# Optimization experiments

Hardware: AMD Instinct MI355X
Metric: run time of the kernel (lower is better)

The kernel has to match this reference:

```python
import jax, jax.numpy as jnp
import numpy as np

BATCH = 2097152
N_BITS = 16

# Differentiable soft gates (exact boolean logic on {0,1} inputs)
def _xor(a, b):
    return a + b - 2.0 * a * b

def _and(a, b):
    return a * b

def _or(a, b):
    return a + b - a * b


def setup_inputs() -> dict:
    key = jax.random.key(0)
    k1, k2 = jax.random.split(key)
    x = jax.random.randint(k1, (BATCH, N_BITS), 0, 2).astype(jnp.float32)
    y = jax.random.randint(k2, (BATCH, N_BITS), 0, 2).astype(jnp.float32)
    return {"x": x, "y": y}


def reference(x, y):
    # Ripple-carry adder: sequential scan over bit positions (LSB first).
    # Full adder with c_in=0 reduces exactly to the half adder used at i==0.
    def step(c_in, ab):
        a, b = ab
        s1 = _xor(a, b)          # half-adder 1 sum
        c1 = _and(a, b)          # half-adder 1 carry
        s = _xor(s1, c_in)       # half-adder 2 sum -> bit output
        c2 = _and(s1, c_in)      # half-adder 2 carry
        c_out = _or(c1, c2)
        return c_out, (s, c_out)

    xT = jnp.swapaxes(x, 0, 1)   # (n_bits, batch)
    yT = jnp.swapaxes(y, 0, 1)
    c0 = jnp.zeros(x.shape[0], dtype=x.dtype)
    _, (s, carry) = jax.lax.scan(step, c0, (xT, yT))
    output = jnp.swapaxes(s, 0, 1)      # (batch, n_bits)
    carry = jnp.swapaxes(carry, 0, 1)   # (batch, n_bits)
    return output, carry
```

## Files before the change

### kernel.cpp

```cpp
#include <hip/hip_runtime.h>


#define BATCH 2097152
#define NB 16

__global__ __launch_bounds__(256) void rca_kernel(
    const uint4* __restrict__ x,
    const uint4* __restrict__ y,
    float4* __restrict__ out)
{
    const int row = blockIdx.x * blockDim.x + threadIdx.x;
    if (row >= BATCH) return;

    const uint4* xp = x + (size_t)row * 4;
    const uint4* yp = y + (size_t)row * 4;

    unsigned int X = 0, Y = 0;
#pragma unroll
    for (int q = 0; q < 4; ++q) {
        uint4 xv = xp[q];
        uint4 yv = yp[q];
        X |= ((xv.x >> 23) & 1u) << (4 * q + 0);
        X |= ((xv.y >> 23) & 1u) << (4 * q + 1);
        X |= ((xv.z >> 23) & 1u) << (4 * q + 2);
        X |= ((xv.w >> 23) & 1u) << (4 * q + 3);
        Y |= ((yv.x >> 23) & 1u) << (4 * q + 0);
        Y |= ((yv.y >> 23) & 1u) << (4 * q + 1);
        Y |= ((yv.z >> 23) & 1u) << (4 * q + 2);
        Y |= ((yv.w >> 23) & 1u) << (4 * q + 3);
    }

    const unsigned int S = X + Y;
    const unsigned int C = (X ^ Y ^ S) >> 1;

    float4* os = out + (size_t)row * 4;
    float4* oc = out + (size_t)BATCH * 4 + (size_t)row * 4;

#pragma unroll
    for (int q = 0; q < 4; ++q) {
        float4 sv, cv;
        sv.x = (float)((S >> (4 * q + 0)) & 1u);
        sv.y = (float)((S >> (4 * q + 1)) & 1u);
        sv.z = (float)((S >> (4 * q + 2)) & 1u);
        sv.w = (float)((S >> (4 * q + 3)) & 1u);
        cv.x = (float)((C >> (4 * q + 0)) & 1u);
        cv.y = (float)((C >> (4 * q + 1)) & 1u);
        cv.z = (float)((C >> (4 * q + 2)) & 1u);
        cv.w = (float)((C >> (4 * q + 3)) & 1u);
        os[q] = sv;
        oc[q] = cv;
    }
}

extern "C" void kernel_launch(void* const* d_in, const int* in_sizes, int n_in,
                              void* d_out, int out_size, void* d_ws, size_t ws_size,
                              hipStream_t stream) {
    const uint4* x = (const uint4*)d_in[0];
    const uint4* y = (const uint4*)d_in[1];
    float4* out = (float4*)d_out;

    const int threads = 256;
    const int blocks = BATCH / threads;
    rca_kernel<<<blocks, threads, 0, stream>>>(x, y, out);
}
```

Baseline: 450.0 us.

## Split each row across four lanes with shuffle-combined bit packing for coalesced access

Each row is now handled by four adjacent threads. Each thread loads one 16-byte chunk of x and y, packs its four bits, and the lanes merge the full 16-bit operands with two xor-shuffles before each writes one float4 of sum and one of carry. This makes consecutive lanes touch consecutive 16-byte chunks instead of 64-byte strided rows, which improves coalescing on a memory-bound kernel. It costs four times as many threads and two cross-lane shuffles per thread.

```diff
diff --git a/kernel.cpp b/kernel.cpp
--- a/kernel.cpp
+++ b/kernel.cpp
@@ -9,47 +9,45 @@
     const uint4* __restrict__ y,
     float4* __restrict__ out)
 {
-    const int row = blockIdx.x * blockDim.x + threadIdx.x;
-    if (row >= BATCH) return;
+    const unsigned int t = blockIdx.x * blockDim.x + threadIdx.x;
+    const int q = (int)(t & 3);
 
-    const uint4* xp = x + (size_t)row * 4;
-    const uint4* yp = y + (size_t)row * 4;
+    const uint4 xv = x[t];
+    const uint4 yv = y[t];
 
-    unsigned int X = 0, Y = 0;
-#pragma unroll
-    for (int q = 0; q < 4; ++q) {
-        uint4 xv = xp[q];
-        uint4 yv = yp[q];
-        X |= ((xv.x >> 23) & 1u) << (4 * q + 0);
-        X |= ((xv.y >> 23) & 1u) << (4 * q + 1);
-        X |= ((xv.z >> 23) & 1u) << (4 * q + 2);
-        X |= ((xv.w >> 23) & 1u) << (4 * q + 3);
-        Y |= ((yv.x >> 23) & 1u) << (4 * q + 0);
-        Y |= ((yv.y >> 23) & 1u) << (4 * q + 1);
-        Y |= ((yv.z >> 23) & 1u) << (4 * q + 2);
-        Y |= ((yv.w >> 23) & 1u) << (4 * q + 3);
-    }
+    unsigned int nx = ((xv.x >> 23) & 1u)
+                    | (((xv.y >> 23) & 1u) << 1)
+                    | (((xv.z >> 23) & 1u) << 2)
+                    | (((xv.w >> 23) & 1u) << 3);
+    unsigned int ny = ((yv.x >> 23) & 1u)
+                    | (((yv.y >> 23) & 1u) << 1)
+                    | (((yv.z >> 23) & 1u) << 2)
+                    | (((yv.w >> 23) & 1u) << 3);
 
+    unsigned int P = (nx << (4 * q)) | (ny << (4 * q + 16));
+    P |= __shfl_xor((int)P, 1);
+    P |= __shfl_xor((int)P, 2);
+
+    const unsigned int X = P & 0xFFFFu;
+    const unsigned int Y = P >> 16;
     const unsigned int S = X + Y;
     const unsigned int C = (X ^ Y ^ S) >> 1;
 
-    float4* os = out + (size_t)row * 4;
-    float4* oc = out + (size_t)BATCH * 4 + (size_t)row * 4;
+    const unsigned int s4 = (S >> (4 * q)) & 0xFu;
+    const unsigned int c4 = (C >> (4 * q)) & 0xFu;
 
-#pragma unroll
-    for (int q = 0; q < 4; ++q) {
-        float4 sv, cv;
-        sv.x = (float)((S >> (4 * q + 0)) & 1u);
-        sv.y = (float)((S >> (4 * q + 1)) & 1u);
-        sv.z = (float)((S >> (4 * q + 2)) & 1u);
-        sv.w = (float)((S >> (4 * q + 3)) & 1u);
-        cv.x = (float)((C >> (4 * q + 0)) & 1u);
-        cv.y = (float)((C >> (4 * q + 1)) & 1u);
-        cv.z = (float)((C >> (4 * q + 2)) & 1u);
-        cv.w = (float)((C >> (4 * q + 3)) & 1u);
-        os[q] = sv;
-        oc[q] = cv;
-    }
+    float4 sv, cv;
+    sv.x = (float)(s4 & 1u);
+    sv.y = (float)((s4 >> 1) & 1u);
+    sv.z = (float)((s4 >> 2) & 1u);
+    sv.w = (float)((s4 >> 3) & 1u);
+    cv.x = (float)(c4 & 1u);
+    cv.y = (float)((c4 >> 1) & 1u);
+    cv.z = (float)((c4 >> 2) & 1u);
+    cv.w = (float)((c4 >> 3) & 1u);
+
+    out[t] = sv;
+    out[t + (size_t)BATCH * 4] = cv;
 }
 
 extern "C" void kernel_launch(void* const* d_in, const int* in_sizes, int n_in,
@@ -60,6 +58,6 @@
     float4* out = (float4*)d_out;
 
     const int threads = 256;
-    const int blocks = BATCH / threads;
+    const int blocks = (BATCH * 4) / threads;
     rca_kernel<<<blocks, threads, 0, stream>>>(x, y, out);
 }
```

Measured after the change: 427.6 us. 1.05x faster.
